# Kernel tuning notes

Hardware: AMD Instinct MI355X
Metric: run time of the kernel (lower is better)

Reference implementation:

```python
import jax, jax.numpy as jnp
import numpy as np

L, H, D, F = 4, 8, 64, 256  # layers, heads, head_dim, FAVOR feature dims (n_dims=256 in source)
DM = H * D                   # d_model = 512
EPS = 1e-6                   # fast_transformers LinearAttention eps


def _ln(x, g, b):
    m = jnp.mean(x, -1, keepdims=True)
    v = jnp.mean((x - m) ** 2, -1, keepdims=True)
    return (x - m) * jax.lax.rsqrt(v + 1e-5) * g + b


def _favor(x, omega):
    # FAVOR+ softmax-kernel feature map. x: [B,S,H,D], omega: [D, F//2]
    x = x * (D ** -0.25)  # x * sqrt(softmax_temp), softmax_temp = 1/sqrt(D)
    u = jnp.einsum('bshd,df->bshf', x, omega)
    h = jnp.sum(x * x, -1, keepdims=True) * 0.5
    return jnp.concatenate([jnp.exp(u - h), jnp.exp(-u - h)], -1) * (F ** -0.5)


def _forward(x, pos, enc_w1, enc_b1, enc_w2, enc_b2, enc_g, enc_b,
             wq, bq, wk, bk, wv, bv, wo, bo, ln1_g, ln1_b,
             w1, b1, w2, b2, ln2_g, ln2_b, omega, cls_w, cls_b, num_graphs):
    B = num_graphs
    N = x.shape[0]
    S = N // B
    # encoder MLP + LayerNorm
    h = jnp.concatenate([x, pos], axis=1)
    h = jax.nn.relu(h @ enc_w1 + enc_b1)
    h = _ln(h @ enc_w2 + enc_b2, enc_g, enc_b)
    h = h.reshape(B, S, DM)
    # fast_transformers post-norm encoder layers with linear (FAVOR) attention
    for l in range(L):
        q = (h @ wq[l] + bq[l]).reshape(B, S, H, D)
        k = (h @ wk[l] + bk[l]).reshape(B, S, H, D)
        v = (h @ wv[l] + bv[l]).reshape(B, S, H, D)
        Q = _favor(q, omega[l])  # [B,S,H,F]
        K = _favor(k, omega[l])
        kv = jnp.einsum('bshf,bshd->bhfd', K, v)                      # associative accumulation
        z = 1.0 / (jnp.einsum('bshf,bhf->bsh', Q, K.sum(axis=1)) + EPS)
        a = jnp.einsum('bshf,bhfd,bsh->bshd', Q, kv, z).reshape(B, S, DM)
        h = _ln(h + a @ wo[l] + bo[l], ln1_g[l], ln1_b[l])            # x = norm1(x + attn)
        y = jax.nn.relu(h @ w1[l] + b1[l]) @ w2[l] + b2[l]            # FFN (relu)
        h = _ln(h + y, ln2_g[l], ln2_b[l])                            # norm2(x + y)
    pooled = h.mean(axis=1)
    return pooled @ cls_w + cls_b


def setup_inputs() -> dict:
    key = jax.random.key(0)
    ks = jax.random.split(key, 16)
    B, S = 16, 1024
    N = B * S

    def w(k, shape):
        return jax.random.normal(k, shape, jnp.float32) * 0.02

    return dict(
        x=jax.random.normal(ks[0], (N, 3), jnp.float32),
        pos=jax.random.normal(ks[1], (N, 3), jnp.float32),
        enc_w1=w(ks[2], (6, DM // 2)), enc_b1=jnp.zeros((DM // 2,), jnp.float32),
        enc_w2=w(ks[3], (DM // 2, DM)), enc_b2=jnp.zeros((DM,), jnp.float32),
        enc_g=jnp.ones((DM,), jnp.float32), enc_b=jnp.zeros((DM,), jnp.float32),
        wq=w(ks[4], (L, DM, DM)), bq=jnp.zeros((L, DM), jnp.float32),
        wk=w(ks[5], (L, DM, DM)), bk=jnp.zeros((L, DM), jnp.float32),
        wv=w(ks[6], (L, DM, DM)), bv=jnp.zeros((L, DM), jnp.float32),
        wo=w(ks[7], (L, DM, DM)), bo=jnp.zeros((L, DM), jnp.float32),
        ln1_g=jnp.ones((L, DM), jnp.float32), ln1_b=jnp.zeros((L, DM), jnp.float32),
        w1=w(ks[8], (L, DM, 2 * DM)), b1=jnp.zeros((L, 2 * DM), jnp.float32),
        w2=w(ks[9], (L, 2 * DM, DM)), b2=jnp.zeros((L, DM), jnp.float32),
        ln2_g=jnp.ones((L, DM), jnp.float32), ln2_b=jnp.zeros((L, DM), jnp.float32),
        omega=jax.random.normal(ks[10], (L, D, F // 2), jnp.float32),
        cls_w=w(ks[11], (DM, 16)), cls_b=jnp.zeros((16,), jnp.float32),
        num_graphs=B,
    )


def reference(x, pos, enc_w1, enc_b1, enc_w2, enc_b2, enc_g, enc_b,
              wq, bq, wk, bk, wv, bv, wo, bo, ln1_g, ln1_b,
              w1, b1, w2, b2, ln2_g, ln2_b, omega, cls_w, cls_b, num_graphs):
    return _forward(x, pos, enc_w1, enc_b1, enc_w2, enc_b2, enc_g, enc_b,
                    wq, bq, wk, bk, wv, bv, wo, bo, ln1_g, ln1_b,
                    w1, b1, w2, b2, ln2_g, ln2_b, omega, cls_w, cls_b, num_graphs)
```

## Files before the change

### kernel.cpp

```cpp
#include <hip/hip_runtime.h>
#include <hip/hip_bf16.h>
#include <math.h>

#define NTOK 16384
#define BATCH 16
#define SEQ 1024
#define DMODEL 512
#define NHEAD 8
#define HDIM 64
#define FDIM 256
#define BH_TOT 128
#define SCALE_QK 0.3535533905932738f
#define SCALE2 0.125f
#define FSCALE 0.0625f

typedef __bf16 bf16x8_t __attribute__((ext_vector_type(8)));
typedef __bf16 bf16x4_t __attribute__((ext_vector_type(4)));
typedef float f32x4_t  __attribute__((ext_vector_type(4)));
typedef unsigned short u16x8 __attribute__((ext_vector_type(8)));
typedef unsigned short u16x4 __attribute__((ext_vector_type(4)));
typedef const __attribute__((address_space(1))) char* gas_t;
typedef __attribute__((address_space(3))) char* las_t;

__device__ __forceinline__ float b2f(unsigned short u) {
    union { unsigned int i; float f; } c; c.i = ((unsigned int)u) << 16; return c.f;
}
__device__ __forceinline__ unsigned short f2bu(float f) {
    __hip_bfloat16 h = __float2bfloat16(f);
    return *(unsigned short*)&h;
}

__global__ void zero_kernel(float* __restrict__ p, int n) {
    int i = blockIdx.x * 256 + threadIdx.x;
    if (i < n) p[i] = 0.f;
}

__global__ __launch_bounds__(256) void convT_batch_kernel(
    const float* __restrict__ W, unsigned short* __restrict__ Wt, int K, int N,
    size_t in_lstride, size_t out_lstride)
{
    int l = blockIdx.z;
    W  += (size_t)l * in_lstride;
    Wt += (size_t)l * out_lstride;
    __shared__ float tile[32][33];
    int k0 = blockIdx.y * 32, n0 = blockIdx.x * 32;
    int t = threadIdx.x;
    int r = t >> 3, c4 = (t & 7) * 4;
    float4 v = *(const float4*)(W + (size_t)(k0 + r) * N + n0 + c4);
    tile[r][c4 + 0] = v.x; tile[r][c4 + 1] = v.y;
    tile[r][c4 + 2] = v.z; tile[r][c4 + 3] = v.w;
    __syncthreads();
    ushort4 o;
    o.x = f2bu(tile[c4 + 0][r]); o.y = f2bu(tile[c4 + 1][r]);
    o.z = f2bu(tile[c4 + 2][r]); o.w = f2bu(tile[c4 + 3][r]);
    *(ushort4*)(Wt + (size_t)(n0 + r) * K + k0 + c4) = o;
}

__global__ __launch_bounds__(256) void omT_kernel(
    const float* __restrict__ om, unsigned short* __restrict__ omT)
{
    int i = blockIdx.x * 256 + threadIdx.x;
    int l = i >> 13, rem = i & 8191;
    int f = rem >> 6, d = rem & 63;
    omT[(size_t)l * 8192 + f * 64 + d] = f2bu(om[(size_t)l * 8192 + d * 128 + f] * SCALE_QK);
}

__global__ __launch_bounds__(256) void enc1_kernel(
    const float* __restrict__ x, const float* __restrict__ pos,
    const float* __restrict__ w1, const float* __restrict__ b1,
    unsigned short* __restrict__ mid)
{
    int row = blockIdx.x, t = threadIdx.x;
    __shared__ float in6[6];
    if (t < 3) in6[t] = x[row * 3 + t];
    else if (t < 6) in6[t] = pos[row * 3 + (t - 3)];
    __syncthreads();
    float acc = b1[t];
#pragma unroll
    for (int j = 0; j < 6; j++) acc += in6[j] * w1[j * 256 + t];
    mid[(size_t)row * 256 + t] = f2bu(fmaxf(acc, 0.f));
}

template<int RELU>
__global__ __launch_bounds__(256) void gemm_bf16_kernel(
    const unsigned short* __restrict__ A, const unsigned short* __restrict__ Bt,
    const float* __restrict__ bias, unsigned short* __restrict__ C,
    int M, int K, int Nc)
{
    __shared__ __align__(16) unsigned short As[128 * 32];
    __shared__ __align__(16) unsigned short Bs[128 * 32];
    const int tid = threadIdx.x;
    const int bm = blockIdx.y * 128, bn = blockIdx.x * 128;
    const int wave = tid >> 6, lane = tid & 63;
    const int wr = (wave >> 1) * 64, wc = (wave & 1) * 64;
    const int lm = lane & 15, lk = (lane >> 4) * 8;

    f32x4_t acc[4][4];
#pragma unroll
    for (int i = 0; i < 4; i++)
#pragma unroll
        for (int j = 0; j < 4; j++)
            acc[i][j] = (f32x4_t){0.f, 0.f, 0.f, 0.f};

    for (int k0 = 0; k0 < K; k0 += 32) {
#pragma unroll
        for (int it = 0; it < 2; ++it) {
            int t = tid + it * 256;
            const unsigned short* gp = A + (size_t)(bm + (t >> 2)) * K + k0 + (t & 3) * 8;
            __builtin_amdgcn_global_load_lds((gas_t)(const char*)gp,
                (las_t)((char*)As + t * 16), 16, 0, 0);
        }
#pragma unroll
        for (int it = 0; it < 2; ++it) {
            int t = tid + it * 256;
            const unsigned short* gp = Bt + (size_t)(bn + (t >> 2)) * K + k0 + (t & 3) * 8;
            __builtin_amdgcn_global_load_lds((gas_t)(const char*)gp,
                (las_t)((char*)Bs + t * 16), 16, 0, 0);
        }
        __syncthreads();
        bf16x8_t af[4], bfr[4];
#pragma unroll
        for (int i = 0; i < 4; i++)
            af[i] = *(const bf16x8_t*)(As + (size_t)(wr + 16 * i + lm) * 32 + lk);
#pragma unroll
        for (int j = 0; j < 4; j++)
            bfr[j] = *(const bf16x8_t*)(Bs + (size_t)(wc + 16 * j + lm) * 32 + lk);
#pragma unroll
        for (int i = 0; i < 4; i++)
#pragma unroll
            for (int j = 0; j < 4; j++)
                acc[i][j] = __builtin_amdgcn_mfma_f32_16x16x32_bf16(af[i], bfr[j], acc[i][j], 0, 0, 0);
        __syncthreads();
    }

    const int col_l = lane & 15;
    const int row_q = (lane >> 4) * 4;
#pragma unroll
    for (int i = 0; i < 4; i++) {
#pragma unroll
        for (int j = 0; j < 4; j++) {
            int gn = bn + wc + 16 * j + col_l;
            float bsv = bias[gn];
            int gm0 = bm + wr + 16 * i + row_q;
#pragma unroll
            for (int r = 0; r < 4; r++) {
                float v = acc[i][j][r] + bsv;
                if (RELU) v = fmaxf(v, 0.f);
                C[(size_t)(gm0 + r) * Nc + gn] = f2bu(v);
            }
        }
    }
}

__global__ __launch_bounds__(256) void gemm_qkv_kernel(
    const unsigned short* __restrict__ A, const unsigned short* __restrict__ Bt,
    const float* __restrict__ bq, const float* __restrict__ bk, const float* __restrict__ bv,
    unsigned short* __restrict__ Q, unsigned short* __restrict__ Kk,
    unsigned short* __restrict__ vT)
{
    __shared__ __align__(16) unsigned short As[128 * 32];
    __shared__ __align__(16) unsigned short Bs[128 * 32];
    const int tid = threadIdx.x;
    const int bm = blockIdx.y * 128, bn = blockIdx.x * 128;
    const int wave = tid >> 6, lane = tid & 63;
    const int wr = (wave >> 1) * 64, wc = (wave & 1) * 64;
    const int lm = lane & 15, lk = (lane >> 4) * 8;
    const int K = DMODEL;

    f32x4_t acc[4][4];
#pragma unroll
    for (int i = 0; i < 4; i++)
#pragma unroll
        for (int j = 0; j < 4; j++)
            acc[i][j] = (f32x4_t){0.f, 0.f, 0.f, 0.f};

    for (int k0 = 0; k0 < K; k0 += 32) {
#pragma unroll
        for (int it = 0; it < 2; ++it) {
            int t = tid + it * 256;
            const unsigned short* gp = A + (size_t)(bm + (t >> 2)) * K + k0 + (t & 3) * 8;
            __builtin_amdgcn_global_load_lds((gas_t)(const char*)gp,
                (las_t)((char*)As + t * 16), 16, 0, 0);
        }
#pragma unroll
        for (int it = 0; it < 2; ++it) {
            int t = tid + it * 256;
            const unsigned short* gp = Bt + (size_t)(bn + (t >> 2)) * K + k0 + (t & 3) * 8;
            __builtin_amdgcn_global_load_lds((gas_t)(const char*)gp,
                (las_t)((char*)Bs + t * 16), 16, 0, 0);
        }
        __syncthreads();
        bf16x8_t af[4], bfr[4];
#pragma unroll
        for (int i = 0; i < 4; i++)
            af[i] = *(const bf16x8_t*)(As + (size_t)(wr + 16 * i + lm) * 32 + lk);
#pragma unroll
        for (int j = 0; j < 4; j++)
            bfr[j] = *(const bf16x8_t*)(Bs + (size_t)(wc + 16 * j + lm) * 32 + lk);
#pragma unroll
        for (int i = 0; i < 4; i++)
#pragma unroll
            for (int j = 0; j < 4; j++)
                acc[i][j] = __builtin_amdgcn_mfma_f32_16x16x32_bf16(af[i], bfr[j], acc[i][j], 0, 0, 0);
        __syncthreads();
    }

    const int sect = bn >> 9;
    const float* bias = (sect == 0) ? bq : (sect == 1) ? bk : bv;
    unsigned short* rowout = (sect == 0) ? Q : Kk;
    const int cb = bn & 511;
    const int col_l = lane & 15;
    const int row_q = (lane >> 4) * 4;
#pragma unroll
    for (int i = 0; i < 4; i++) {
#pragma unroll
        for (int j = 0; j < 4; j++) {
            int cn = cb + wc + 16 * j + col_l;
            float bsv = bias[cn];
            int gm0 = bm + wr + 16 * i + row_q;
            if (sect < 2) {
#pragma unroll
                for (int r = 0; r < 4; r++)
                    rowout[(size_t)(gm0 + r) * DMODEL + cn] = f2bu(acc[i][j][r] + bsv);
            } else {
                int bb_ = gm0 >> 10, ss = gm0 & 1023;
                int hh_ = cn >> 6, dd = cn & 63;
                u16x4 o4;
#pragma unroll
                for (int r = 0; r < 4; r++) o4[r] = f2bu(acc[i][j][r] + bsv);
                *(u16x4*)(vT + (((size_t)(bb_ * NHEAD + hh_) * HDIM + dd) * SEQ + ss)) = o4;
            }
        }
    }
}

__global__ __launch_bounds__(256) void favor_k_kv_kernel(
    const unsigned short* __restrict__ Kx,
    const unsigned short* __restrict__ vT,
    const unsigned short* __restrict__ omT,
    float* __restrict__ kvpart,
    float* __restrict__ ksum)
{
    const int bid = blockIdx.x;
    const int chunk = bid & 3;
    const int bh = bid >> 2;
    const int b = bh >> 3, h = bh & 7;
    const int tid = threadIdx.x;
    const int wave = tid >> 6, lane = tid & 63;
    const int lm = lane & 15, lk = (lane >> 4) * 8;
    const int col_l = lane & 15, quad4 = (lane >> 4) * 4;
    const int wr = wave * 64;
    const int m0 = wave * 16;

    __shared__ __align__(16) unsigned short xs[64 * 72];
    __shared__ __align__(16) unsigned short phiT[256 * 72];
    __shared__ float hs[64];

    f32x4_t acc_kv[4][4];
#pragma unroll
    for (int i = 0; i < 4; i++)
#pragma unroll
        for (int j = 0; j < 4; j++)
            acc_kv[i][j] = (f32x4_t){0.f, 0.f, 0.f, 0.f};
    float ks_acc = 0.f;

    const unsigned short* vbase = vT + (size_t)bh * HDIM * SEQ;

    for (int st = 0; st < 4; ++st) {
        int s0 = chunk * 256 + st * 64;
        __syncthreads();
#pragma unroll
        for (int it = 0; it < 2; ++it) {
            int idx = tid + it * 256;
            int r = idx >> 3, c = (idx & 7) * 8;
            *(u16x8*)&xs[r * 72 + c] =
                *(const u16x8*)(Kx + (size_t)(b * SEQ + s0 + r) * DMODEL + h * HDIM + c);
        }
        __syncthreads();
        {
            int token = tid >> 2, seg = (tid & 3) * 16;
            float p = 0.f;
#pragma unroll
            for (int j = 0; j < 16; j++) {
                float xv = b2f(xs[token * 72 + seg + j]);
                p += xv * xv;
            }
            p += __shfl_down(p, 2, 4);
            p += __shfl_down(p, 1, 4);
            if ((tid & 3) == 0) hs[token] = 0.5f * SCALE2 * p;
        }
        f32x4_t acc[8];
#pragma unroll
        for (int j = 0; j < 8; j++) acc[j] = (f32x4_t){0.f, 0.f, 0.f, 0.f};
#pragma unroll
        for (int ks = 0; ks < 2; ks++) {
            bf16x8_t af = *(const bf16x8_t*)&xs[(m0 + lm) * 72 + ks * 32 + lk];
#pragma unroll
            for (int j = 0; j < 8; j++) {
                bf16x8_t bfr = *(const bf16x8_t*)(omT + (size_t)(j * 16 + lm) * 64 + ks * 32 + lk);
                acc[j] = __builtin_amdgcn_mfma_f32_16x16x32_bf16(af, bfr, acc[j], 0, 0, 0);
            }
        }
        __syncthreads();
#pragma unroll
        for (int j = 0; j < 8; j++) {
            int f = j * 16 + col_l;
#pragma unroll
            for (int r = 0; r < 4; r++) {
                int m = m0 + quad4 + r;
                float u = acc[j][r], hh = hs[m];
                phiT[f * 72 + m]         = f2bu(__expf(u - hh) * FSCALE);
                phiT[(f + 128) * 72 + m] = f2bu(__expf(-u - hh) * FSCALE);
            }
        }
        __syncthreads();
        {
            const unsigned short* row = &phiT[tid * 72];
#pragma unroll
            for (int mm = 0; mm < 64; mm += 8) {
                u16x8 v = *(const u16x8*)(row + mm);
#pragma unroll
                for (int e = 0; e < 8; e++) ks_acc += b2f(v[e]);
            }
        }
#pragma unroll
        for (int ks = 0; ks < 2; ks++) {
            bf16x8_t af[4], bfr[4];
#pragma unroll
            for (int i = 0; i < 4; i++)
                af[i] = *(const bf16x8_t*)&phiT[(wr + 16 * i + lm) * 72 + ks * 32 + lk];
#pragma unroll
            for (int j = 0; j < 4; j++)
                bfr[j] = *(const bf16x8_t*)(vbase + (size_t)(16 * j + lm) * SEQ + s0 + ks * 32 + lk);
#pragma unroll
            for (int i = 0; i < 4; i++)
#pragma unroll
                for (int j = 0; j < 4; j++)
                    acc_kv[i][j] = __builtin_amdgcn_mfma_f32_16x16x32_bf16(af[i], bfr[j], acc_kv[i][j], 0, 0, 0);
        }
    }

    float* kp = kvpart + ((size_t)chunk * BH_TOT + bh) * HDIM * FDIM;
#pragma unroll
    for (int i = 0; i < 4; i++) {
#pragma unroll
        for (int j = 0; j < 4; j++) {
            int d = 16 * j + col_l;
            int f0 = wr + 16 * i + quad4;
            *(f32x4_t*)(kp + (size_t)d * FDIM + f0) = acc_kv[i][j];
        }
    }
    atomicAdd(&ksum[(size_t)bh * FDIM + tid], ks_acc);
}

__global__ __launch_bounds__(256) void reduce_kv_kernel(
    const float* __restrict__ in, unsigned short* __restrict__ out)
{
    const size_t STRIDE = (size_t)BH_TOT * HDIM * FDIM;
    size_t i = (size_t)blockIdx.x * 256 + threadIdx.x;
    out[i] = f2bu(in[i] + in[i + STRIDE] + in[i + 2 * STRIDE] + in[i + 3 * STRIDE]);
}

__global__ __launch_bounds__(256) void favor_q_attn_kernel(
    const unsigned short* __restrict__ Qx,
    const unsigned short* __restrict__ omT,
    const unsigned short* __restrict__ kvT,
    const float* __restrict__ ksum,
    unsigned short* __restrict__ outX)
{
    const int bid = blockIdx.x;
    const int sc = bid & 15;
    const int bh = bid >> 4;
    const int b = bh >> 3, h = bh & 7;
    const int s0 = sc * 64;
    const int tid = threadIdx.x;
    const int wave = tid >> 6, lane = tid & 63;
    const int lm = lane & 15, lk = (lane >> 4) * 8;
    const int col_l = lane & 15, quad4 = (lane >> 4) * 4;
    const int m0 = wave * 16;

    __shared__ __align__(16) unsigned short xs[64 * 72];
    __shared__ __align__(8)  unsigned short phis[64 * 268];
    __shared__ float hs[64];
    __shared__ float zz[64];
    __shared__ float kss[256];

#pragma unroll
    for (int it = 0; it < 2; ++it) {
        int idx = tid + it * 256;
        int r = idx >> 3, c = (idx & 7) * 8;
        *(u16x8*)&xs[r * 72 + c] =
            *(const u16x8*)(Qx + (size_t)(b * SEQ + s0 + r) * DMODEL + h * HDIM + c);
    }
    kss[tid] = ksum[(size_t)bh * FDIM + tid];
    __syncthreads();

    {
        int token = tid >> 2, seg = (tid & 3) * 16;
        float p = 0.f;
#pragma unroll
        for (int j = 0; j < 16; j++) {
            float xv = b2f(xs[token * 72 + seg + j]);
            p += xv * xv;
        }
        p += __shfl_down(p, 2, 4);
        p += __shfl_down(p, 1, 4);
        if ((tid & 3) == 0) hs[token] = 0.5f * SCALE2 * p;
    }
    f32x4_t acc[8];
#pragma unroll
    for (int j = 0; j < 8; j++) acc[j] = (f32x4_t){0.f, 0.f, 0.f, 0.f};
#pragma unroll
    for (int ks = 0; ks < 2; ks++) {
        bf16x8_t af = *(const bf16x8_t*)&xs[(m0 + lm) * 72 + ks * 32 + lk];
#pragma unroll
        for (int j = 0; j < 8; j++) {
            bf16x8_t bfr = *(const bf16x8_t*)(omT + (size_t)(j * 16 + lm) * 64 + ks * 32 + lk);
            acc[j] = __builtin_amdgcn_mfma_f32_16x16x32_bf16(af, bfr, acc[j], 0, 0, 0);
        }
    }
    __syncthreads();
#pragma unroll
    for (int j = 0; j < 8; j++) {
        int f = j * 16 + col_l;
#pragma unroll
        for (int r = 0; r < 4; r++) {
            int m = m0 + quad4 + r;
            float u = acc[j][r], hh = hs[m];
            phis[m * 268 + f]       = f2bu(__expf(u - hh) * FSCALE);
            phis[m * 268 + 128 + f] = f2bu(__expf(-u - hh) * FSCALE);
        }
    }
    __syncthreads();
    {
        int m = tid >> 2, q = tid & 3;
        float zp = 0.f;
#pragma unroll
        for (int kchunk = 0; kchunk < 8; kchunk++) {
            int fp = q * 8 + kchunk * 32;
            u16x4 v0 = *(const u16x4*)&phis[m * 268 + fp];
            u16x4 v1 = *(const u16x4*)&phis[m * 268 + fp + 4];
#pragma unroll
            for (int e = 0; e < 4; e++) {
                zp += b2f(v0[e]) * kss[fp + e];
                zp += b2f(v1[e]) * kss[fp + 4 + e];
            }
        }
        zp += __shfl_down(zp, 2, 4);
        zp += __shfl_down(zp, 1, 4);
        if (q == 0) zz[m] = 1.f / (zp + 1e-6f);
    }
    __syncthreads();
    const unsigned short* kvbase = kvT + (size_t)bh * HDIM * FDIM;
    f32x4_t acc_o[4];
#pragma unroll
    for (int j = 0; j < 4; j++) acc_o[j] = (f32x4_t){0.f, 0.f, 0.f, 0.f};
#pragma unroll
    for (int k0 = 0; k0 < FDIM; k0 += 32) {
        bf16x4_t alo = *(const bf16x4_t*)&phis[(m0 + lm) * 268 + k0 + lk];
        bf16x4_t ahi = *(const bf16x4_t*)&phis[(m0 + lm) * 268 + k0 + lk + 4];
        bf16x8_t af;
#pragma unroll
        for (int e = 0; e < 4; e++) { af[e] = alo[e]; af[4 + e] = ahi[e]; }
#pragma unroll
        for (int j = 0; j < 4; j++) {
            bf16x8_t bfr = *(const bf16x8_t*)(kvbase + (size_t)(16 * j + lm) * FDIM + k0 + lk);
            acc_o[j] = __builtin_amdgcn_mfma_f32_16x16x32_bf16(af, bfr, acc_o[j], 0, 0, 0);
        }
    }
#pragma unroll
    for (int r = 0; r < 4; r++) {
        int m = m0 + quad4 + r;
        float zv = zz[m];
        int s = s0 + m;
#pragma unroll
        for (int j = 0; j < 4; j++) {
            int d = 16 * j + col_l;
            outX[(size_t)(b * SEQ + s) * DMODEL + h * HDIM + d] = f2bu(acc_o[j][r] * zv);
        }
    }
}

template<int HAS_RES>
__global__ __launch_bounds__(512) void add_ln_kernel(
    const unsigned short* __restrict__ res16, const unsigned short* __restrict__ tin16,
    const float* __restrict__ g, const float* __restrict__ bb,
    unsigned short* __restrict__ out16)
{
    int row = blockIdx.x, t = threadIdx.x;
    size_t idx = (size_t)row * DMODEL + t;
    float val = b2f(tin16[idx]);
    if (HAS_RES) val += b2f(res16[idx]);
    float s1 = val, s2 = val * val;
#pragma unroll
    for (int off = 32; off; off >>= 1) {
        s1 += __shfl_down(s1, off, 64);
        s2 += __shfl_down(s2, off, 64);
    }
    __shared__ float w1s[8], w2s[8];
    int wid = t >> 6, lane = t & 63;
    if (lane == 0) { w1s[wid] = s1; w2s[wid] = s2; }
    __syncthreads();
    if (t == 0) {
        float a1 = 0.f, a2 = 0.f;
#pragma unroll
        for (int i = 0; i < 8; i++) { a1 += w1s[i]; a2 += w2s[i]; }
        w1s[0] = a1 * (1.f / DMODEL);
        w2s[0] = a2 * (1.f / DMODEL);
    }
    __syncthreads();
    float m = w1s[0];
    float var = w2s[0] - m * m;
    float r = rsqrtf(var + 1e-5f);
    out16[idx] = f2bu((val - m) * r * g[t] + bb[t]);
}

__global__ __launch_bounds__(256) void pool_part_kernel(
    const unsigned short* __restrict__ h16, float* __restrict__ pbuf)
{
    int blk = blockIdx.x;
    int b = blk >> 4, ch = blk & 15;
    int t = threadIdx.x;
    int d0 = t * 2;
    float a0 = 0.f, a1 = 0.f;
    const unsigned short* base = h16 + ((size_t)(b * SEQ + ch * 64) * DMODEL) + d0;
#pragma unroll 4
    for (int s = 0; s < 64; s++) {
        ushort2 v = *(const ushort2*)(base + (size_t)s * DMODEL);
        a0 += b2f(v.x); a1 += b2f(v.y);
    }
    *(float2*)(pbuf + (size_t)blk * DMODEL + d0) = make_float2(a0, a1);
}

__global__ __launch_bounds__(512) void cls_kernel(
    const float* __restrict__ pbuf, const float* __restrict__ cls_w,
    const float* __restrict__ cls_b, float* __restrict__ out)
{
    int b = blockIdx.x, t = threadIdx.x;
    float s = 0.f;
#pragma unroll
    for (int c = 0; c < 16; c++) s += pbuf[(size_t)(b * 16 + c) * DMODEL + t];
    __shared__ float pooled[DMODEL];
    pooled[t] = s * (1.f / SEQ);
    __syncthreads();
    if (t < 16) {
        float acc = cls_b[t];
        for (int c = 0; c < DMODEL; c++) acc += pooled[c] * cls_w[c * 16 + t];
        out[b * 16 + t] = acc;
    }
}

extern "C" void kernel_launch(void* const* d_in, const int* in_sizes, int n_in,
                              void* d_out, int out_size, void* d_ws, size_t ws_size,
                              hipStream_t stream)
{
    const float* x      = (const float*)d_in[0];
    const float* pos    = (const float*)d_in[1];
    const float* enc_w1 = (const float*)d_in[2];
    const float* enc_b1 = (const float*)d_in[3];
    const float* enc_w2 = (const float*)d_in[4];
    const float* enc_b2 = (const float*)d_in[5];
    const float* enc_g  = (const float*)d_in[6];
    const float* enc_bb = (const float*)d_in[7];
    const float* wq = (const float*)d_in[8];
    const float* bq = (const float*)d_in[9];
    const float* wk = (const float*)d_in[10];
    const float* bk = (const float*)d_in[11];
    const float* wv = (const float*)d_in[12];
    const float* bv = (const float*)d_in[13];
    const float* wo = (const float*)d_in[14];
    const float* bo = (const float*)d_in[15];
    const float* ln1_g = (const float*)d_in[16];
    const float* ln1_b = (const float*)d_in[17];
    const float* w1 = (const float*)d_in[18];
    const float* b1 = (const float*)d_in[19];
    const float* w2 = (const float*)d_in[20];
    const float* b2 = (const float*)d_in[21];
    const float* ln2_g = (const float*)d_in[22];
    const float* ln2_b = (const float*)d_in[23];
    const float* omega = (const float*)d_in[24];
    const float* cls_w = (const float*)d_in[25];
    const float* cls_b = (const float*)d_in[26];
    float* out = (float*)d_out;

    const int N = NTOK;
    const int BH = BH_TOT;

    char* p = (char*)d_ws;
    unsigned short* qb16 = (unsigned short*)p; p += (size_t)N * DMODEL * 2;
    unsigned short* kb16 = (unsigned short*)p; p += (size_t)N * DMODEL * 2;
    unsigned short* vT16 = (unsigned short*)p; p += (size_t)N * DMODEL * 2;
    unsigned short* h16  = (unsigned short*)p; p += (size_t)N * DMODEL * 2;
    unsigned short* mid16 = (unsigned short*)p; p += (size_t)N * 1024 * 2;
    unsigned short* attn16 = (unsigned short*)p; p += (size_t)N * DMODEL * 2;
    float* kvpart = (float*)p;                 p += (size_t)4 * BH * HDIM * FDIM * 4;
    unsigned short* kvT16 = (unsigned short*)p; p += (size_t)BH * HDIM * FDIM * 2;
    float* ksb = (float*)p;                    p += (size_t)BH * FDIM * 4;
    float* pbuf = (float*)p;                   p += (size_t)BATCH * 16 * DMODEL * 4;
    unsigned short* enc_w2t = (unsigned short*)p; p += (size_t)256 * 512 * 2;
    unsigned short* wqkvt = (unsigned short*)p; p += (size_t)4 * 1536 * 512 * 2;
    unsigned short* wot = (unsigned short*)p;  p += (size_t)4 * 512 * 512 * 2;
    unsigned short* w1t = (unsigned short*)p;  p += (size_t)4 * 512 * 1024 * 2;
    unsigned short* w2t = (unsigned short*)p;  p += (size_t)4 * 1024 * 512 * 2;
    unsigned short* omT = (unsigned short*)p;  p += (size_t)4 * 128 * 64 * 2;

    convT_batch_kernel<<<dim3(16, 8, 1), 256, 0, stream>>>(enc_w2, enc_w2t, 256, 512, 0, 0);
    convT_batch_kernel<<<dim3(16, 16, 4), 256, 0, stream>>>(wq, wqkvt,            512, 512, 262144, 786432);
    convT_batch_kernel<<<dim3(16, 16, 4), 256, 0, stream>>>(wk, wqkvt + 262144,   512, 512, 262144, 786432);
    convT_batch_kernel<<<dim3(16, 16, 4), 256, 0, stream>>>(wv, wqkvt + 524288,   512, 512, 262144, 786432);
    convT_batch_kernel<<<dim3(16, 16, 4), 256, 0, stream>>>(wo, wot, 512, 512, 262144, 262144);
    convT_batch_kernel<<<dim3(32, 16, 4), 256, 0, stream>>>(w1, w1t, 512, 1024, 524288, 524288);
    convT_batch_kernel<<<dim3(16, 32, 4), 256, 0, stream>>>(w2, w2t, 1024, 512, 524288, 524288);
    omT_kernel<<<128, 256, 0, stream>>>(omega, omT);

    enc1_kernel<<<N, 256, 0, stream>>>(x, pos, enc_w1, enc_b1, mid16);
    gemm_bf16_kernel<0><<<dim3(4, 128), 256, 0, stream>>>(mid16, enc_w2t, enc_b2, qb16, N, 256, 512);
    add_ln_kernel<0><<<N, 512, 0, stream>>>(nullptr, qb16, enc_g, enc_bb, h16);

    for (int l = 0; l < 4; l++) {
        const unsigned short* omT_l = omT + (size_t)l * 8192;
        gemm_qkv_kernel<<<dim3(12, 128), 256, 0, stream>>>(
            h16, wqkvt + (size_t)l * 786432,
            bq + l * DMODEL, bk + l * DMODEL, bv + l * DMODEL,
            qb16, kb16, vT16);
        zero_kernel<<<BH * FDIM / 256, 256, 0, stream>>>(ksb, BH * FDIM);
        favor_k_kv_kernel<<<BH * 4, 256, 0, stream>>>(kb16, vT16, omT_l, kvpart, ksb);
        reduce_kv_kernel<<<BH * HDIM * FDIM / 256, 256, 0, stream>>>(kvpart, kvT16);
        favor_q_attn_kernel<<<BH * 16, 256, 0, stream>>>(qb16, omT_l, kvT16, ksb, attn16);
        gemm_bf16_kernel<0><<<dim3(4, 128), 256, 0, stream>>>(attn16, wot + (size_t)l * 262144, bo + l * DMODEL, qb16, N, 512, 512);
        add_ln_kernel<1><<<N, 512, 0, stream>>>(h16, qb16, ln1_g + l * DMODEL, ln1_b + l * DMODEL, h16);
        gemm_bf16_kernel<1><<<dim3(8, 128), 256, 0, stream>>>(h16, w1t + (size_t)l * 524288, b1 + l * 1024, mid16, N, 512, 1024);
        gemm_bf16_kernel<0><<<dim3(4, 128), 256, 0, stream>>>(mid16, w2t + (size_t)l * 524288, b2 + l * DMODEL, qb16, N, 1024, 512);
        add_ln_kernel<1><<<N, 512, 0, stream>>>(h16, qb16, ln2_g + l * DMODEL, ln2_b + l * DMODEL, h16);
    }

    pool_part_kernel<<<BATCH * 16, 256, 0, stream>>>(h16, pbuf);
    cls_kernel<<<BATCH, 512, 0, stream>>>(pbuf, cls_w, cls_b, out);
}
```

Measured before the change: 1.258 ms.

## Remap GEMM blocks per XCD and load FAVOR inputs directly into registers

The GEMM kernels now use a 1D grid with a block-index remap, so that consecutive blocks on the same XCD share an A row-tile and get better L2 reuse. The FAVOR K and Q kernels drop the LDS staging of the input rows: each lane loads its MFMA fragment straight from global memory and computes the squared norm with cross-lane shuffles. The Q attention kernel also fuses the normalizer computation into the feature-map pass and processes the positive and negative feature halves one after the other, which halves the phi shared buffer. In exchange it adds extra barriers and recomputes the exp for the second half.

```diff
diff --git a/kernel.cpp b/kernel.cpp
--- a/kernel.cpp
+++ b/kernel.cpp
@@ -15,7 +15,6 @@
 #define FSCALE 0.0625f
 
 typedef __bf16 bf16x8_t __attribute__((ext_vector_type(8)));
-typedef __bf16 bf16x4_t __attribute__((ext_vector_type(4)));
 typedef float f32x4_t  __attribute__((ext_vector_type(4)));
 typedef unsigned short u16x8 __attribute__((ext_vector_type(8)));
 typedef unsigned short u16x4 __attribute__((ext_vector_type(4)));
@@ -28,6 +27,9 @@
 __device__ __forceinline__ unsigned short f2bu(float f) {
     __hip_bfloat16 h = __float2bfloat16(f);
     return *(unsigned short*)&h;
+}
+__device__ __forceinline__ bf16x8_t u2b8(u16x8 u) {
+    union { u16x8 a; bf16x8_t b; } c; c.a = u; return c.b;
 }
 
 __global__ void zero_kernel(float* __restrict__ p, int n) {
@@ -85,12 +87,15 @@
 __global__ __launch_bounds__(256) void gemm_bf16_kernel(
     const unsigned short* __restrict__ A, const unsigned short* __restrict__ Bt,
     const float* __restrict__ bias, unsigned short* __restrict__ C,
-    int M, int K, int Nc)
+    int M, int K, int Nc, int nx)
 {
     __shared__ __align__(16) unsigned short As[128 * 32];
     __shared__ __align__(16) unsigned short Bs[128 * 32];
     const int tid = threadIdx.x;
-    const int bm = blockIdx.y * 128, bn = blockIdx.x * 128;
+    const int id = blockIdx.x;
+    const int xcd = id & 7, slot = id >> 3;
+    const int bm = ((slot / nx) * 8 + xcd) * 128;
+    const int bn = (slot % nx) * 128;
     const int wave = tid >> 6, lane = tid & 63;
     const int wr = (wave >> 1) * 64, wc = (wave & 1) * 64;
     const int lm = lane & 15, lk = (lane >> 4) * 8;
@@ -161,7 +166,10 @@
     __shared__ __align__(16) unsigned short As[128 * 32];
     __shared__ __align__(16) unsigned short Bs[128 * 32];
     const int tid = threadIdx.x;
-    const int bm = blockIdx.y * 128, bn = blockIdx.x * 128;
+    const int id = blockIdx.x;
+    const int xcd = id & 7, slot = id >> 3;
+    const int bm = ((slot / 12) * 8 + xcd) * 128;
+    const int bn = (slot % 12) * 128;
     const int wave = tid >> 6, lane = tid & 63;
     const int wr = (wave >> 1) * 64, wc = (wave & 1) * 64;
     const int lm = lane & 15, lk = (lane >> 4) * 8;
@@ -247,14 +255,13 @@
     const int b = bh >> 3, h = bh & 7;
     const int tid = threadIdx.x;
     const int wave = tid >> 6, lane = tid & 63;
-    const int lm = lane & 15, lk = (lane >> 4) * 8;
-    const int col_l = lane & 15, quad4 = (lane >> 4) * 4;
+    const int lm = lane & 15, q = lane >> 4, lk = q * 8;
+    const int quad4 = q * 4;
     const int wr = wave * 64;
     const int m0 = wave * 16;
 
-    __shared__ __align__(16) unsigned short xs[64 * 72];
     __shared__ __align__(16) unsigned short phiT[256 * 72];
-    __shared__ float hs[64];
+    __shared__ float hsh[64];
 
     f32x4_t acc_kv[4][4];
 #pragma unroll
@@ -268,47 +275,38 @@
 
     for (int st = 0; st < 4; ++st) {
         int s0 = chunk * 256 + st * 64;
+        const unsigned short* krow = Kx + (size_t)(b * SEQ + s0 + m0 + lm) * DMODEL + h * HDIM;
+        u16x8 xu0 = *(const u16x8*)(krow + lk);
+        u16x8 xu1 = *(const u16x8*)(krow + 32 + lk);
+        float p = 0.f;
+#pragma unroll
+        for (int e = 0; e < 8; e++) {
+            float a = b2f(xu0[e]), c = b2f(xu1[e]);
+            p += a * a + c * c;
+        }
+        p += __shfl_xor(p, 16, 64);
+        p += __shfl_xor(p, 32, 64);
         __syncthreads();
-#pragma unroll
-        for (int it = 0; it < 2; ++it) {
-            int idx = tid + it * 256;
-            int r = idx >> 3, c = (idx & 7) * 8;
-            *(u16x8*)&xs[r * 72 + c] =
-                *(const u16x8*)(Kx + (size_t)(b * SEQ + s0 + r) * DMODEL + h * HDIM + c);
+        if (q == 0) hsh[m0 + lm] = 0.5f * SCALE2 * p;
+        f32x4_t acc[8];
+#pragma unroll
+        for (int j = 0; j < 8; j++) acc[j] = (f32x4_t){0.f, 0.f, 0.f, 0.f};
+        bf16x8_t af0 = u2b8(xu0), af1 = u2b8(xu1);
+#pragma unroll
+        for (int j = 0; j < 8; j++) {
+            bf16x8_t b0 = *(const bf16x8_t*)(omT + (size_t)(j * 16 + lm) * 64 + lk);
+            acc[j] = __builtin_amdgcn_mfma_f32_16x16x32_bf16(af0, b0, acc[j], 0, 0, 0);
+            bf16x8_t b1 = *(const bf16x8_t*)(omT + (size_t)(j * 16 + lm) * 64 + 32 + lk);
+            acc[j] = __builtin_amdgcn_mfma_f32_16x16x32_bf16(af1, b1, acc[j], 0, 0, 0);
         }
         __syncthreads();
-        {
-            int token = tid >> 2, seg = (tid & 3) * 16;
-            float p = 0.f;
-#pragma unroll
-            for (int j = 0; j < 16; j++) {
-                float xv = b2f(xs[token * 72 + seg + j]);
-                p += xv * xv;
-            }
-            p += __shfl_down(p, 2, 4);
-            p += __shfl_down(p, 1, 4);
-            if ((tid & 3) == 0) hs[token] = 0.5f * SCALE2 * p;
-        }
-        f32x4_t acc[8];
-#pragma unroll
-        for (int j = 0; j < 8; j++) acc[j] = (f32x4_t){0.f, 0.f, 0.f, 0.f};
-#pragma unroll
-        for (int ks = 0; ks < 2; ks++) {
-            bf16x8_t af = *(const bf16x8_t*)&xs[(m0 + lm) * 72 + ks * 32 + lk];
-#pragma unroll
-            for (int j = 0; j < 8; j++) {
-                bf16x8_t bfr = *(const bf16x8_t*)(omT + (size_t)(j * 16 + lm) * 64 + ks * 32 + lk);
-                acc[j] = __builtin_amdgcn_mfma_f32_16x16x32_bf16(af, bfr, acc[j], 0, 0, 0);
-            }
-        }
-        __syncthreads();
 #pragma unroll
         for (int j = 0; j < 8; j++) {
-            int f = j * 16 + col_l;
+            int f = j * 16 + lm;
 #pragma unroll
             for (int r = 0; r < 4; r++) {
                 int m = m0 + quad4 + r;
-                float u = acc[j][r], hh = hs[m];
+                float u = acc[j][r], hh = hsh[m];
                 phiT[f * 72 + m]         = f2bu(__expf(u - hh) * FSCALE);
                 phiT[(f + 128) * 72 + m] = f2bu(__expf(-u - hh) * FSCALE);
             }
@@ -345,7 +343,7 @@
     for (int i = 0; i < 4; i++) {
 #pragma unroll
         for (int j = 0; j < 4; j++) {
-            int d = 16 * j + col_l;
+            int d = 16 * j + lm;
             int f0 = wr + 16 * i + quad4;
             *(f32x4_t*)(kp + (size_t)d * FDIM + f0) = acc_kv[i][j];
         }
@@ -375,107 +373,113 @@
     const int s0 = sc * 64;
     const int tid = threadIdx.x;
     const int wave = tid >> 6, lane = tid & 63;
-    const int lm = lane & 15, lk = (lane >> 4) * 8;
-    const int col_l = lane & 15, quad4 = (lane >> 4) * 4;
+    const int lm = lane & 15, q = lane >> 4, lk = q * 8;
+    const int quad4 = q * 4;
     const int m0 = wave * 16;
 
-    __shared__ __align__(16) unsigned short xs[64 * 72];
-    __shared__ __align__(8)  unsigned short phis[64 * 268];
-    __shared__ float hs[64];
-    __shared__ float zz[64];
+    __shared__ __align__(16) unsigned short phis[64 * 136];
     __shared__ float kss[256];
-
-#pragma unroll
-    for (int it = 0; it < 2; ++it) {
-        int idx = tid + it * 256;
-        int r = idx >> 3, c = (idx & 7) * 8;
-        *(u16x8*)&xs[r * 72 + c] =
-            *(const u16x8*)(Qx + (size_t)(b * SEQ + s0 + r) * DMODEL + h * HDIM + c);
-    }
+    __shared__ float hsh[64];
+    __shared__ float zzs[64];
+
     kss[tid] = ksum[(size_t)bh * FDIM + tid];
-    __syncthreads();
-
-    {
-        int token = tid >> 2, seg = (tid & 3) * 16;
-        float p = 0.f;
-#pragma unroll
-        for (int j = 0; j < 16; j++) {
-            float xv = b2f(xs[token * 72 + seg + j]);
-            p += xv * xv;
-        }
-        p += __shfl_down(p, 2, 4);
-        p += __shfl_down(p, 1, 4);
-        if ((tid & 3) == 0) hs[token] = 0.5f * SCALE2 * p;
-    }
+
+    const unsigned short* qrow = Qx + (size_t)(b * SEQ + s0 + m0 + lm) * DMODEL + h * HDIM;
+    u16x8 xu0 = *(const u16x8*)(qrow + lk);
+    u16x8 xu1 = *(const u16x8*)(qrow + 32 + lk);
+    float p = 0.f;
+#pragma unroll
+    for (int e = 0; e < 8; e++) {
+        float a = b2f(xu0[e]), c = b2f(xu1[e]);
+        p += a * a + c * c;
+    }
+    p += __shfl_xor(p, 16, 64);
+    p += __shfl_xor(p, 32, 64);
+    if (q == 0) hsh[m0 + lm] = 0.5f * SCALE2 * p;
+
     f32x4_t acc[8];
 #pragma unroll
     for (int j = 0; j < 8; j++) acc[j] = (f32x4_t){0.f, 0.f, 0.f, 0.f};
-#pragma unroll
-    for (int ks = 0; ks < 2; ks++) {
-        bf16x8_t af = *(const bf16x8_t*)&xs[(m0 + lm) * 72 + ks * 32 + lk];
-#pragma unroll
-        for (int j = 0; j < 8; j++) {
-            bf16x8_t bfr = *(const bf16x8_t*)(omT + (size_t)(j * 16 + lm) * 64 + ks * 32 + lk);
-            acc[j] = __builtin_amdgcn_mfma_f32_16x16x32_bf16(af, bfr, acc[j], 0, 0, 0);
-        }
-    }
-    __syncthreads();
+    bf16x8_t af0 = u2b8(xu0), af1 = u2b8(xu1);
 #pragma unroll
     for (int j = 0; j < 8; j++) {
-        int f = j * 16 + col_l;
+        bf16x8_t b0 = *(const bf16x8_t*)(omT + (size_t)(j * 16 + lm) * 64 + lk);
+        acc[j] = __builtin_amdgcn_mfma_f32_16x16x32_bf16(af0, b0, acc[j], 0, 0, 0);
+        bf16x8_t b1 = *(const bf16x8_t*)(omT + (size_t)(j * 16 + lm) * 64 + 32 + lk);
+        acc[j] = __builtin_amdgcn_mfma_f32_16x16x32_bf16(af1, b1, acc[j], 0, 0, 0);
+    }
+    __syncthreads();
+
+    float zp[4] = {0.f, 0.f, 0.f, 0.f};
+#pragma unroll
+    for (int j = 0; j < 8; j++) {
+        int f = j * 16 + lm;
+        float ksp = kss[f], ksm = kss[128 + f];
 #pragma unroll
         for (int r = 0; r < 4; r++) {
             int m = m0 + quad4 + r;
-            float u = acc[j][r], hh = hs[m];
-            phis[m * 268 + f]       = f2bu(__expf(u - hh) * FSCALE);
-            phis[m * 268 + 128 + f] = f2bu(__expf(-u - hh) * FSCALE);
-        }
-    }
-    __syncthreads();
-    {
-        int m = tid >> 2, q = tid & 3;
-        float zp = 0.f;
-#pragma unroll
-        for (int kchunk = 0; kchunk < 8; kchunk++) {
-            int fp = q * 8 + kchunk * 32;
-            u16x4 v0 = *(const u16x4*)&phis[m * 268 + fp];
-            u16x4 v1 = *(const u16x4*)&phis[m * 268 + fp + 4];
-#pragma unroll
-            for (int e = 0; e < 4; e++) {
-                zp += b2f(v0[e]) * kss[fp + e];
-                zp += b2f(v1[e]) * kss[fp + 4 + e];
-            }
-        }
-        zp += __shfl_down(zp, 2, 4);
-        zp += __shfl_down(zp, 1, 4);
-        if (q == 0) zz[m] = 1.f / (zp + 1e-6f);
-    }
-    __syncthreads();
+            float u = acc[j][r], hh = hsh[m];
+            float pp = __expf(u - hh) * FSCALE;
+            float pm = __expf(-u - hh) * FSCALE;
+            phis[m * 136 + f] = f2bu(pp);
+            zp[r] += pp * ksp + pm * ksm;
+        }
+    }
+#pragma unroll
+    for (int off = 1; off < 16; off <<= 1) {
+        zp[0] += __shfl_xor(zp[0], off, 64);
+        zp[1] += __shfl_xor(zp[1], off, 64);
+        zp[2] += __shfl_xor(zp[2], off, 64);
+        zp[3] += __shfl_xor(zp[3], off, 64);
+    }
+    if (lm == 0) {
+#pragma unroll
+        for (int r = 0; r < 4; r++)
+            zzs[m0 + quad4 + r] = 1.f / (zp[r] + 1e-6f);
+    }
+    __syncthreads();
+
     const unsigned short* kvbase = kvT + (size_t)bh * HDIM * FDIM;
     f32x4_t acc_o[4];
 #pragma unroll
     for (int j = 0; j < 4; j++) acc_o[j] = (f32x4_t){0.f, 0.f, 0.f, 0.f};
 #pragma unroll
-    for (int k0 = 0; k0 < FDIM; k0 += 32) {
-        bf16x4_t alo = *(const bf16x4_t*)&phis[(m0 + lm) * 268 + k0 + lk];
-        bf16x4_t ahi = *(const bf16x4_t*)&phis[(m0 + lm) * 268 + k0 + lk + 4];
-        bf16x8_t af;
-#pragma unroll
-        for (int e = 0; e < 4; e++) { af[e] = alo[e]; af[4 + e] = ahi[e]; }
+    for (int k0 = 0; k0 < 128; k0 += 32) {
+        bf16x8_t af = *(const bf16x8_t*)&phis[(m0 + lm) * 136 + k0 + lk];
 #pragma unroll
         for (int j = 0; j < 4; j++) {
             bf16x8_t bfr = *(const bf16x8_t*)(kvbase + (size_t)(16 * j + lm) * FDIM + k0 + lk);
             acc_o[j] = __builtin_amdgcn_mfma_f32_16x16x32_bf16(af, bfr, acc_o[j], 0, 0, 0);
         }
     }
+    __syncthreads();
+#pragma unroll
+    for (int j = 0; j < 8; j++) {
+        int f = j * 16 + lm;
+#pragma unroll
+        for (int r = 0; r < 4; r++) {
+            int m = m0 + quad4 + r;
+            phis[m * 136 + f] = f2bu(__expf(-acc[j][r] - hsh[m]) * FSCALE);
+        }
+    }
+    __syncthreads();
+#pragma unroll
+    for (int k0 = 0; k0 < 128; k0 += 32) {
+        bf16x8_t af = *(const bf16x8_t*)&phis[(m0 + lm) * 136 + k0 + lk];
+#pragma unroll
+        for (int j = 0; j < 4; j++) {
+            bf16x8_t bfr = *(const bf16x8_t*)(kvbase + (size_t)(16 * j + lm) * FDIM + 128 + k0 + lk);
+            acc_o[j] = __builtin_amdgcn_mfma_f32_16x16x32_bf16(af, bfr, acc_o[j], 0, 0, 0);
+        }
+    }
 #pragma unroll
     for (int r = 0; r < 4; r++) {
         int m = m0 + quad4 + r;
-        float zv = zz[m];
+        float zv = zzs[m];
         int s = s0 + m;
 #pragma unroll
         for (int j = 0; j < 4; j++) {
-            int d = 16 * j + col_l;
+            int d = 16 * j + lm;
             outX[(size_t)(b * SEQ + s) * DMODEL + h * HDIM + d] = f2bu(acc_o[j][r] * zv);
         }
     }
@@ -614,12 +618,12 @@
     omT_kernel<<<128, 256, 0, stream>>>(omega, omT);
 
     enc1_kernel<<<N, 256, 0, stream>>>(x, pos, enc_w1, enc_b1, mid16);
-    gemm_bf16_kernel<0><<<dim3(4, 128), 256, 0, stream>>>(mid16, enc_w2t, enc_b2, qb16, N, 256, 512);
+    gemm_bf16_kernel<0><<<4 * 128, 256, 0, stream>>>(mid16, enc_w2t, enc_b2, qb16, N, 256, 512, 4);
     add_ln_kernel<0><<<N, 512, 0, stream>>>(nullptr, qb16, enc_g, enc_bb, h16);
 
     for (int l = 0; l < 4; l++) {
         const unsigned short* omT_l = omT + (size_t)l * 8192;
-        gemm_qkv_kernel<<<dim3(12, 128), 256, 0, stream>>>(
+        gemm_qkv_kernel<<<12 * 128, 256, 0, stream>>>(
             h16, wqkvt + (size_t)l * 786432,
             bq + l * DMODEL, bk + l * DMODEL, bv + l * DMODEL,
             qb16, kb16, vT16);
@@ -627,10 +631,10 @@
         favor_k_kv_kernel<<<BH * 4, 256, 0, stream>>>(kb16, vT16, omT_l, kvpart, ksb);
         reduce_kv_kernel<<<BH * HDIM * FDIM / 256, 256, 0, stream>>>(kvpart, kvT16);
         favor_q_attn_kernel<<<BH * 16, 256, 0, stream>>>(qb16, omT_l, kvT16, ksb, attn16);
-        gemm_bf16_kernel<0><<<dim3(4, 128), 256, 0, stream>>>(attn16, wot + (size_t)l * 262144, bo + l * DMODEL, qb16, N, 512, 512);
+        gemm_bf16_kernel<0><<<4 * 128, 256, 0, stream>>>(attn16, wot + (size_t)l * 262144, bo + l * DMODEL, qb16, N, 512, 512, 4);
         add_ln_kernel<1><<<N, 512, 0, stream>>>(h16, qb16, ln1_g + l * DMODEL, ln1_b + l * DMODEL, h16);
-        gemm_bf16_kernel<1><<<dim3(8, 128), 256, 0, stream>>>(h16, w1t + (size_t)l * 524288, b1 + l * 1024, mid16, N, 512, 1024);
-        gemm_bf16_kernel<0><<<dim3(4, 128), 256, 0, stream>>>(mid16, w2t + (size_t)l * 524288, b2 + l * DMODEL, qb16, N, 1024, 512);
+        gemm_bf16_kernel<1><<<8 * 128, 256, 0, stream>>>(h16, w1t + (size_t)l * 524288, b1 + l * 1024, mid16, N, 512, 1024, 8);
+        gemm_bf16_kernel<0><<<4 * 128, 256, 0, stream>>>(mid16, w2t + (size_t)l * 524288, b2 + l * DMODEL, qb16, N, 1024, 512, 4);
         add_ln_kernel<1><<<N, 512, 0, stream>>>(h16, qb16, ln2_g + l * DMODEL, ln2_b + l * DMODEL, h16);
     }
 
```

New measurement: 1.198 ms. 1.05x faster.
